# Performance work log

Hardware: AMD Instinct MI355X
Metric: run time of the kernel (lower is better)

Reference implementation:

```python
import jax, jax.numpy as jnp
import numpy as np

V, H, B, T = 32000, 512, 32, 64


def _gru(x, h0, Wih, Whh, bih, bhh):
    """PyTorch-style GRU, batch_first. x: [B,T,D], h0: [B,H]. Returns ([B,T,H], [B,H])."""
    # precompute input projections for all timesteps: [B,T,3H]
    xp = jnp.einsum('btd,gd->btg', x, Wih) + bih

    def step(h, xp_t):
        hp = h @ Whh.T + bhh                      # [B,3H]
        xr, xz, xn = jnp.split(xp_t, 3, axis=-1)
        hr, hz, hn = jnp.split(hp, 3, axis=-1)
        r = jax.nn.sigmoid(xr + hr)
        z = jax.nn.sigmoid(xz + hz)
        n = jnp.tanh(xn + r * hn)
        h_new = (1.0 - z) * n + z * h
        return h_new, h_new

    h_last, ys = jax.lax.scan(step, h0, jnp.swapaxes(xp, 0, 1))
    return jnp.swapaxes(ys, 0, 1), h_last


def setup_inputs() -> dict:
    key = jax.random.key(0)
    ks = jax.random.split(key, 12)
    s_emb = 1.0  # nn.Embedding default N(0,1)
    s_gru = 1.0 / np.sqrt(H)  # nn.GRU uniform(-1/sqrt(H), 1/sqrt(H))
    u = lambda k, shape, s: jax.random.uniform(k, shape, jnp.float32, -s, s)
    return {
        'input_seqs': jax.random.randint(ks[0], (B, T), 0, V),
        'target_seqs': jax.random.randint(ks[1], (B, T), 0, V),
        'enc_emb': jax.random.normal(ks[2], (V, H), jnp.float32) * s_emb,
        'enc_Wih': u(ks[3], (3 * H, H), s_gru),
        'enc_Whh': u(ks[4], (3 * H, H), s_gru),
        'enc_bih': u(ks[5], (3 * H,), s_gru),
        'enc_bhh': u(ks[6], (3 * H,), s_gru),
        'dec_emb': jax.random.normal(ks[7], (V, H), jnp.float32) * s_emb,
        'dec_Wih': u(ks[8], (3 * H, 2 * H), s_gru),
        'dec_Whh': u(ks[9], (3 * H, H), s_gru),
        'dec_bih': u(ks[10], (3 * H,), s_gru),
        'dec_bhh': u(ks[11], (3 * H,), s_gru),
        'out_W': u(jax.random.fold_in(key, 100), (V, H), s_gru),
        'out_b': u(jax.random.fold_in(key, 101), (V,), s_gru),
    }


def reference(input_seqs, target_seqs, enc_emb, enc_Wih, enc_Whh, enc_bih, enc_bhh,
              dec_emb, dec_Wih, dec_Whh, dec_bih, dec_bhh, out_W, out_b):
    b = input_seqs.shape[0]
    h0 = jnp.zeros((b, H), jnp.float32)
    # encoder: embed + single-layer GRU; thought = final hidden
    enc_x = enc_emb[input_seqs]                                  # [B,T,H]
    _, thought = _gru(enc_x, h0, enc_Wih, enc_Whh, enc_bih, enc_bhh)  # [B,H]
    # decoder: concat embedded target with broadcast thought along time
    dec_x = dec_emb[target_seqs]                                 # [B,T,H]
    t = dec_x.shape[1]
    rnn_in = jnp.concatenate([dec_x, jnp.broadcast_to(thought[:, None, :], (b, t, H))], axis=-1)
    rnn_in = jax.nn.relu(rnn_in)
    dec_out, _ = _gru(rnn_in, h0, dec_Wih, dec_Whh, dec_bih, dec_bhh)  # [B,T,H]
    logits = jnp.einsum('bth,vh->btv', dec_out, out_W) + out_b
    return jax.nn.log_softmax(logits, axis=-1)
```

## Files before the change

kernel.cpp:

```cpp
#include <hip/hip_runtime.h>
#include <hip/hip_bf16.h>
#include <cstdint>
#include <cstddef>

namespace {

constexpr int Hh = 512;
constexpr int G3 = 1536;
constexpr int Bb = 32;
constexpr int Tt = 64;
constexpr int Vv = 32000;

typedef __attribute__((ext_vector_type(8))) short short8;
typedef __attribute__((ext_vector_type(4))) float f32x4;
typedef unsigned long long ull;

__device__ __forceinline__ unsigned bf16bits(float f) {
  union { __hip_bfloat16 h; unsigned short u; } c;
  c.h = __float2bfloat16(f);
  return (unsigned)c.u;
}

__device__ __forceinline__ void gl_lds16(const void* g, void* l) {
  __builtin_amdgcn_global_load_lds(
      (const __attribute__((address_space(1))) unsigned int*)g,
      (__attribute__((address_space(3))) unsigned int*)l, 16, 0, 0);
}

__device__ __forceinline__ void cvt_range(const float* __restrict__ src,
                                          __hip_bfloat16* __restrict__ dst, int i, int n4) {
  if (i >= n4) return;
  float4 v = ((const float4*)src)[i];
  union { __hip_bfloat16 h[4]; uint2 u; } o;
  o.h[0] = __float2bfloat16(v.x);
  o.h[1] = __float2bfloat16(v.y);
  o.h[2] = __float2bfloat16(v.z);
  o.h[3] = __float2bfloat16(v.w);
  ((uint2*)dst)[i] = o.u;
}

__device__ __forceinline__ void pack_whh_core(const float* __restrict__ Whh,
                                              uint2* __restrict__ P, int k0, int i0) {
  __shared__ float tw[3][32][65];
  const int t = threadIdx.x;
  const int kk = t & 63, r4 = t >> 6;
  for (int ri = r4; ri < 96; ri += 4) {
    const int g = ri >> 5, ii = ri & 31;
    tw[g][ii][kk] = Whh[(size_t)(g * 512 + i0 + ii) * 512 + k0 + kk];
  }
  __syncthreads();
  const int ii = t & 31, kq = t >> 5;
  for (int k2 = kq; k2 < 64; k2 += 8) {
    unsigned rb = bf16bits(tw[0][ii][k2]);
    unsigned zb = bf16bits(tw[1][ii][k2]);
    unsigned nb = bf16bits(tw[2][ii][k2]);
    P[(size_t)(k0 + k2) * 512 + i0 + ii] = make_uint2((zb << 16) | rb, nb);
  }
}

__global__ __launch_bounds__(256) void prep_k(
    const float* __restrict__ enc_Wih, __hip_bfloat16* __restrict__ encWih_bf,
    const float* __restrict__ dec_Wih, __hip_bfloat16* __restrict__ decWih_bf,
    const float* __restrict__ enc_Whh, uint2* __restrict__ whhB_e,
    const float* __restrict__ dec_Whh, uint2* __restrict__ whhB_d,
    uint4* __restrict__ hTagZero) {
  const int blk = blockIdx.x;
  if (blk < 768) {
    cvt_range(enc_Wih, encWih_bf, blk * 256 + threadIdx.x, 1536 * 512 / 4);
  } else if (blk < 2304) {
    cvt_range(dec_Wih, decWih_bf, (blk - 768) * 256 + threadIdx.x, 1536 * 1024 / 4);
  } else if (blk < 2432) {
    const int b = blk - 2304;
    pack_whh_core(enc_Whh, whhB_e, (b & 7) * 64, (b >> 3) * 32);
  } else if (blk < 2560) {
    const int b = blk - 2432;
    pack_whh_core(dec_Whh, whhB_d, (b & 7) * 64, (b >> 3) * 32);
  } else {
    const int i = (blk - 2560) * 256 + threadIdx.x;
    hTagZero[i] = make_uint4(0u, 0u, 0u, 0u);
  }
}

__global__ void embed_k(const int* __restrict__ idx, const float* __restrict__ emb,
                        __hip_bfloat16* __restrict__ outp, int do_relu) {
  int row = blockIdx.x;
  int r = idx[row];
  float4 v = ((const float4*)(emb + (size_t)r * Hh))[threadIdx.x];
  if (do_relu) {
    v.x = fmaxf(v.x, 0.f); v.y = fmaxf(v.y, 0.f);
    v.z = fmaxf(v.z, 0.f); v.w = fmaxf(v.w, 0.f);
  }
  union { __hip_bfloat16 h[4]; uint2 u; } o;
  o.h[0] = __float2bfloat16(v.x);
  o.h[1] = __float2bfloat16(v.y);
  o.h[2] = __float2bfloat16(v.z);
  o.h[3] = __float2bfloat16(v.w);
  ((uint2*)(outp + (size_t)row * Hh))[threadIdx.x] = o.u;
}

__global__ __launch_bounds__(256) void gemm_bf16_k(
    const __hip_bfloat16* __restrict__ A,
    const __hip_bfloat16* __restrict__ B,
    float* __restrict__ C,
    __hip_bfloat16* __restrict__ Cbf,
    int lda, int ldb, int ldc, int K,
    const float* __restrict__ bias1,
    float2* __restrict__ partials,
    int ntm) {
  __shared__ __align__(16) char smem[32768];
  auto sA = (__hip_bfloat16(*)[64])smem;
  auto sB = (__hip_bfloat16(*)[64])(smem + 16384);

  const unsigned nwg = gridDim.x, gid = blockIdx.x;
  const unsigned q = nwg >> 3, r8 = nwg & 7, xc = gid & 7, jj = gid >> 3;
  const unsigned wg = (xc < r8 ? xc * (q + 1) : r8 * (q + 1) + (xc - r8) * q) + jj;
  const int m0 = (int)(wg % (unsigned)ntm) << 7;
  const int n0 = (int)(wg / (unsigned)ntm) << 7;

  const int tid = threadIdx.x;
  const int l = tid & 63, w = tid >> 6;
  const int wm = (w & 1) << 6, wn = (w >> 1) << 6;
  const int lr = l & 15;
  const int lk = (l >> 4) << 3;
  const int lrow = (w << 3) + (l >> 3);
  const int lcol = (l & 7) << 3;

  f32x4 acc[4][4];
  #pragma unroll
  for (int i = 0; i < 4; ++i)
    #pragma unroll
    for (int j = 0; j < 4; ++j) acc[i][j] = {0.f, 0.f, 0.f, 0.f};

  for (int k0 = 0; k0 < K; k0 += 64) {
    #pragma unroll
    for (int rr = 0; rr < 4; ++rr) {
      gl_lds16(A + (size_t)(m0 + (rr << 5) + lrow) * lda + k0 + lcol, &sA[(rr << 5) + (w << 3)][0]);
      gl_lds16(B + (size_t)(n0 + (rr << 5) + lrow) * ldb + k0 + lcol, &sB[(rr << 5) + (w << 3)][0]);
    }
    __syncthreads();
    #pragma unroll
    for (int kk = 0; kk < 64; kk += 32) {
      short8 aF[4], bF[4];
      #pragma unroll
      for (int ms = 0; ms < 4; ++ms) aF[ms] = *(const short8*)(&sA[wm + (ms << 4) + lr][kk + lk]);
      #pragma unroll
      for (int ns = 0; ns < 4; ++ns) bF[ns] = *(const short8*)(&sB[wn + (ns << 4) + lr][kk + lk]);
      #pragma unroll
      for (int ms = 0; ms < 4; ++ms)
        #pragma unroll
        for (int ns = 0; ns < 4; ++ns)
          acc[ms][ns] = __builtin_amdgcn_mfma_f32_16x16x32_bf16(aF[ms], bF[ns], acc[ms][ns], 0, 0, 0);
    }
    __syncthreads();
  }

  float* sg = (float*)smem + w * 1088;
  const int r2w = l >> 4;
  const int cw = l & 15;
  const int rbase = r2w << 2;
  #pragma unroll
  for (int ms = 0; ms < 4; ++ms) {
    #pragma unroll
    for (int ns = 0; ns < 4; ++ns)
      #pragma unroll
      for (int r = 0; r < 4; ++r) sg[(rbase + r) * 68 + (ns << 4) + lr] = acc[ms][ns][r];
    #pragma unroll
    for (int qq = 0; qq < 4; ++qq) {
      const int srow2 = (qq << 2) + r2w;
      float4 v = *(const float4*)&sg[srow2 * 68 + (cw << 2)];
      const int row = m0 + wm + (ms << 4) + srow2;
      const int col = n0 + wn + (cw << 2);
      if (bias1) {
        float4 b1 = *(const float4*)&bias1[col];
        v.x += b1.x; v.y += b1.y; v.z += b1.z; v.w += b1.w;
      }
      if (partials) {
        float m4 = fmaxf(fmaxf(v.x, v.y), fmaxf(v.z, v.w));
        #pragma unroll
        for (int hop = 1; hop < 16; hop <<= 1) m4 = fmaxf(m4, __shfl_xor(m4, hop));
        float e = __expf(v.x - m4) + __expf(v.y - m4) + __expf(v.z - m4) + __expf(v.w - m4);
        #pragma unroll
        for (int hop = 1; hop < 16; hop <<= 1) e += __shfl_xor(e, hop);
        if (cw == 0) partials[(size_t)row * 500 + ((n0 >> 6) + (wn >> 6))] = make_float2(m4, e);
        union { __hip_bfloat16 h[4]; uint2 u; } o;
        o.h[0] = __float2bfloat16(v.x);
        o.h[1] = __float2bfloat16(v.y);
        o.h[2] = __float2bfloat16(v.z);
        o.h[3] = __float2bfloat16(v.w);
        *(uint2*)&Cbf[(size_t)row * ldc + col] = o.u;
      } else {
        *(float4*)&C[(size_t)row * ldc + col] = v;
      }
    }
  }
}

__device__ __forceinline__ void gru_core(
    const int slice, const int bg,
    const float* __restrict__ xp, const uint2* __restrict__ whhB,
    const float* __restrict__ bhh,
    ull* __restrict__ hTag, __hip_bfloat16* __restrict__ dec_out,
    char* smem,
    const ull* __restrict__ thoughtTag,
    const float* __restrict__ decWih,
    const float* __restrict__ dec_bih) {
  float* sH = (float*)smem;
  float* sRed = (float*)(smem + 8192);
  const int tid = threadIdx.x;
  const int i0 = slice << 5;
  const int il = tid & 31, kc = tid >> 5;
  const int kb0 = kc << 5;

  float wrF[32], wzF[32], wnF[32];
  {
    const uint2* wp = whhB + i0 + il;
    #pragma unroll
    for (int k4 = 0; k4 < 8; ++k4) {
      #pragma unroll
      for (int j = 0; j < 4; ++j) {
        const int idx = (k4 << 2) + j;
        uint2 wv = wp[(size_t)(kb0 + idx) << 9];
        wrF[idx] = __uint_as_float(wv.x << 16);
        wzF[idx] = __uint_as_float(wv.x & 0xffff0000u);
        wnF[idx] = __uint_as_float(wv.y << 16);
      }
    }
  }

  float bh_r = 0.f, bh_z = 0.f, bh_n = 0.f;
  float tpr = 0.f, tpz = 0.f, tpn = 0.f;
  int gi = 0, bb = 0;
  if (tid < 128) {
    const int b = tid >> 5, i2 = tid & 31;
    gi = i0 + i2;
    bb = (bg << 2) + b;
    bh_r = bhh[gi]; bh_z = bhh[512 + gi]; bh_n = bhh[1024 + gi];
  }
  if (thoughtTag) {
    #pragma unroll
    for (int j = 0; j < 4; ++j) {
      ull v = __hip_atomic_load(thoughtTag + ((size_t)bg << 11) + (j << 9) + tid,
                                __ATOMIC_RELAXED, __HIP_MEMORY_SCOPE_AGENT);
      sH[(j << 9) + tid] = fmaxf(__uint_as_float((unsigned)v), 0.f);
    }
    __syncthreads();
    if (tid < 384) {
      const int b = tid / 96, j = tid % 96;
      const int g = j >> 5, i2 = j & 31;
      const int row = g * 512 + i0 + i2;
      const float4* w4 = (const float4*)(decWih + (size_t)row * 1024 + 512);
      const float* th = &sH[b << 9];
      float s = dec_bih[row];
      #pragma unroll 4
      for (int k = 0; k < 128; ++k) {
        float4 w = w4[k];
        float4 t4 = *(const float4*)&th[k << 2];
        s += w.x * t4.x + w.y * t4.y + w.z * t4.z + w.w * t4.w;
      }
      sRed[tid] = s;
    }
    __syncthreads();
    if (tid < 128) {
      const int b = tid >> 5, i2 = tid & 31;
      tpr = sRed[b * 96 + i2];
      tpz = sRed[b * 96 + 32 + i2];
      tpn = sRed[b * 96 + 64 + i2];
    }
    __syncthreads();
  }

  #pragma unroll 1
  for (int t = 0; t < Tt; ++t) {
    {
      const ull* hb = hTag + ((size_t)(t & 1) << 14) + ((size_t)bg << 11);
      #pragma unroll
      for (int j = 0; j < 4; ++j) {
        const ull* p = hb + (j << 9) + tid;
        ull v = __hip_atomic_load(p, __ATOMIC_RELAXED, __HIP_MEMORY_SCOPE_AGENT);
        while ((unsigned)(v >> 32) != (unsigned)t) {
          __builtin_amdgcn_s_sleep(1);
          v = __hip_atomic_load(p, __ATOMIC_RELAXED, __HIP_MEMORY_SCOPE_AGENT);
        }
        sH[(j << 9) + tid] = __uint_as_float((unsigned)v);
      }
    }
    __syncthreads();

    float a[12];
    #pragma unroll
    for (int v = 0; v < 12; ++v) a[v] = 0.f;
    #pragma unroll
    for (int k4 = 0; k4 < 8; ++k4) {
      const int kb = kb0 + (k4 << 2);
      float4 hv0 = *(const float4*)&sH[kb];
      float4 hv1 = *(const float4*)&sH[512 + kb];
      float4 hv2 = *(const float4*)&sH[1024 + kb];
      float4 hv3 = *(const float4*)&sH[1536 + kb];
      const float* h0p = (const float*)&hv0;
      const float* h1p = (const float*)&hv1;
      const float* h2p = (const float*)&hv2;
      const float* h3p = (const float*)&hv3;
      #pragma unroll
      for (int j = 0; j < 4; ++j) {
        const int idx = (k4 << 2) + j;
        const float wr = wrF[idx], wz = wzF[idx], wn = wnF[idx];
        a[0]  = fmaf(wr, h0p[j], a[0]);  a[1]  = fmaf(wz, h0p[j], a[1]);  a[2]  = fmaf(wn, h0p[j], a[2]);
        a[3]  = fmaf(wr, h1p[j], a[3]);  a[4]  = fmaf(wz, h1p[j], a[4]);  a[5]  = fmaf(wn, h1p[j], a[5]);
        a[6]  = fmaf(wr, h2p[j], a[6]);  a[7]  = fmaf(wz, h2p[j], a[7]);  a[8]  = fmaf(wn, h2p[j], a[8]);
        a[9]  = fmaf(wr, h3p[j], a[9]);  a[10] = fmaf(wz, h3p[j], a[10]); a[11] = fmaf(wn, h3p[j], a[11]);
      }
    }
    {
      float* red = &sRed[tid * 13];
      #pragma unroll
      for (int v = 0; v < 12; ++v) red[v] = a[v];
    }
    __syncthreads();

    if (tid < 128) {
      const int b = tid >> 5, i2 = tid & 31;
      float s0 = 0.f, s1 = 0.f, s2 = 0.f;
      #pragma unroll
      for (int kc2 = 0; kc2 < 16; ++kc2) {
        const float* rp = &sRed[(kc2 * 32 + i2) * 13 + b * 3];
        s0 += rp[0]; s1 += rp[1]; s2 += rp[2];
      }
      const float hr = s0 + bh_r;
      const float hz = s1 + bh_z;
      const float hn = s2 + bh_n;
      const size_t m = (size_t)bb * Tt + t;
      const float xr = xp[m * G3 + gi] + tpr;
      const float xz = xp[m * G3 + 512 + gi] + tpz;
      const float xn = xp[m * G3 + 1024 + gi] + tpn;
      const float rg = 1.f / (1.f + __expf(-(xr + hr)));
      const float zg = 1.f / (1.f + __expf(-(xz + hz)));
      const float ng = tanhf(xn + rg * hn);
      const float hnew = (1.f - zg) * ng + zg * sH[(b << 9) + gi];
      ull* dst = hTag + ((size_t)((t + 1) & 1) << 14) + ((size_t)bb << 9) + gi;
      __hip_atomic_store(dst, ((ull)(unsigned)(t + 1) << 32) | (ull)__float_as_uint(hnew),
                         __ATOMIC_RELAXED, __HIP_MEMORY_SCOPE_AGENT);
      if (dec_out) dec_out[((size_t)m << 9) + gi] = __float2bfloat16(hnew);
    }
    __syncthreads();
  }
}

__device__ __forceinline__ void gemm_tile_core(
    const int tid, const int m0, const int n0,
    const __hip_bfloat16* __restrict__ A, const __hip_bfloat16* __restrict__ B,
    float* __restrict__ C, int lda, int ldb, int ldc, int K, char* smem) {
  auto sA = (__hip_bfloat16(*)[64])smem;
  auto sB = (__hip_bfloat16(*)[64])(smem + 16384);
  const int l = tid & 63, w = tid >> 6;
  const int wm = (w & 1) << 6, wn = (w >> 1) << 6;
  const int lr = l & 15;
  const int lk = (l >> 4) << 3;
  const int lrow = (w << 3) + (l >> 3);
  const int lcol = (l & 7) << 3;

  f32x4 acc[4][4];
  #pragma unroll
  for (int i = 0; i < 4; ++i)
    #pragma unroll
    for (int j = 0; j < 4; ++j) acc[i][j] = {0.f, 0.f, 0.f, 0.f};

  for (int k0 = 0; k0 < K; k0 += 64) {
    #pragma unroll
    for (int rr = 0; rr < 4; ++rr) {
      gl_lds16(A + (size_t)(m0 + (rr << 5) + lrow) * lda + k0 + lcol, &sA[(rr << 5) + (w << 3)][0]);
      gl_lds16(B + (size_t)(n0 + (rr << 5) + lrow) * ldb + k0 + lcol, &sB[(rr << 5) + (w << 3)][0]);
    }
    __syncthreads();
    #pragma unroll
    for (int kk = 0; kk < 64; kk += 32) {
      short8 aF[4], bF[4];
      #pragma unroll
      for (int ms = 0; ms < 4; ++ms) aF[ms] = *(const short8*)(&sA[wm + (ms << 4) + lr][kk + lk]);
      #pragma unroll
      for (int ns = 0; ns < 4; ++ns) bF[ns] = *(const short8*)(&sB[wn + (ns << 4) + lr][kk + lk]);
      #pragma unroll
      for (int ms = 0; ms < 4; ++ms)
        #pragma unroll
        for (int ns = 0; ns < 4; ++ns)
          acc[ms][ns] = __builtin_amdgcn_mfma_f32_16x16x32_bf16(aF[ms], bF[ns], acc[ms][ns], 0, 0, 0);
    }
    __syncthreads();
  }

  float* sg = (float*)smem + w * 1088;
  const int r2w = l >> 4;
  const int cw = l & 15;
  const int rbase = r2w << 2;
  #pragma unroll
  for (int ms = 0; ms < 4; ++ms) {
    #pragma unroll
    for (int ns = 0; ns < 4; ++ns)
      #pragma unroll
      for (int r = 0; r < 4; ++r) sg[(rbase + r) * 68 + (ns << 4) + lr] = acc[ms][ns][r];
    #pragma unroll
    for (int qq = 0; qq < 4; ++qq) {
      const int srow2 = (qq << 2) + r2w;
      float4 v = *(const float4*)&sg[srow2 * 68 + (cw << 2)];
      *(float4*)&C[(size_t)(m0 + wm + (ms << 4) + srow2) * ldc + n0 + wn + (cw << 2)] = v;
    }
  }
}

__global__ __launch_bounds__(512, 1) void enc_fused_k(
    const float* __restrict__ enc_xp, const uint2* __restrict__ whhB_e,
    const float* __restrict__ enc_bhh, ull* __restrict__ hTag_e,
    const __hip_bfloat16* __restrict__ decX_bf, const __hip_bfloat16* __restrict__ decWih_bf,
    float* __restrict__ dec_xp,
    const float* __restrict__ out_W, __hip_bfloat16* __restrict__ outW_bf) {
  __shared__ __align__(16) char smem[65536];
  const int blk = blockIdx.x;
  if (blk < 128) {
    gru_core(blk & 15, blk >> 4, enc_xp, whhB_e, enc_bhh, hTag_e, nullptr, smem,
             nullptr, nullptr, nullptr);
  } else if (blk < 224) {
    const int half = threadIdx.x >> 8;
    const int tile = ((blk - 128) << 1) + half;
    const int m0 = (tile & 15) << 7;
    const int n0 = (tile >> 4) << 7;
    gemm_tile_core(threadIdx.x & 255, m0, n0, decX_bf, decWih_bf, dec_xp,
                   512, 1024, G3, 512, smem + (half << 15));
  } else {
    const int n4 = Vv * Hh / 4;
    for (int i = ((blk - 224) << 9) + threadIdx.x; i < n4; i += 16 * 512) {
      float4 v = ((const float4*)out_W)[i];
      union { __hip_bfloat16 h[4]; uint2 u; } o;
      o.h[0] = __float2bfloat16(v.x);
      o.h[1] = __float2bfloat16(v.y);
      o.h[2] = __float2bfloat16(v.z);
      o.h[3] = __float2bfloat16(v.w);
      ((uint2*)outW_bf)[i] = o.u;
    }
  }
}

__global__ __launch_bounds__(512, 1) void gru_dec_k(
    const float* __restrict__ xp, const uint2* __restrict__ whhB,
    const float* __restrict__ bhh,
    const ull* __restrict__ thoughtTag,
    const float* __restrict__ decWih, const float* __restrict__ dec_bih,
    ull* __restrict__ hTag, __hip_bfloat16* __restrict__ dec_out) {
  __shared__ __align__(16) char smem[34816];
  gru_core(blockIdx.x & 15, blockIdx.x >> 4, xp, whhB, bhh, hTag, dec_out, smem,
           thoughtTag, decWih, dec_bih);
}

__global__ __launch_bounds__(256) void lsm_final_k(float* __restrict__ X,
                                                   const float2* __restrict__ P) {
  const int row = blockIdx.x;
  const int tid = threadIdx.x;
  float m = -3.4e38f, s = 0.f;
  for (int j = tid; j < 500; j += 256) {
    float2 p = P[(size_t)row * 500 + j];
    if (p.x > m) { s = s * __expf(m - p.x) + p.y; m = p.x; }
    else         { s += p.y * __expf(p.x - m); }
  }
  #pragma unroll
  for (int off2 = 32; off2 > 0; off2 >>= 1) {
    float mo = __shfl_down(m, off2);
    float so = __shfl_down(s, off2);
    float M = fmaxf(m, mo);
    s = s * __expf(m - M) + so * __expf(mo - M);
    m = M;
  }
  __shared__ float sm[4], ss[4];
  if ((tid & 63) == 0) { sm[tid >> 6] = m; ss[tid >> 6] = s; }
  __syncthreads();
  const float M4 = fmaxf(fmaxf(sm[0], sm[1]), fmaxf(sm[2], sm[3]));
  const float S = ss[0] * __expf(sm[0] - M4) + ss[1] * __expf(sm[1] - M4) +
                  ss[2] * __expf(sm[2] - M4) + ss[3] * __expf(sm[3] - M4);
  const float c = M4 + __logf(S);
  float4* p4 = (float4*)(X + (size_t)row * Vv);
  for (int j = tid; j < Vv / 4; j += 256) {
    float4 v = p4[j];
    v.x -= c; v.y -= c; v.z -= c; v.w -= c;
    p4[j] = v;
  }
}

__global__ __launch_bounds__(256) void lsm_final2_k(float* __restrict__ X,
                                                    const __hip_bfloat16* __restrict__ L,
                                                    const float2* __restrict__ P) {
  const int row = blockIdx.x;
  const int tid = threadIdx.x;
  float m = -3.4e38f, s = 0.f;
  for (int j = tid; j < 500; j += 256) {
    float2 p = P[(size_t)row * 500 + j];
    if (p.x > m) { s = s * __expf(m - p.x) + p.y; m = p.x; }
    else         { s += p.y * __expf(p.x - m); }
  }
  #pragma unroll
  for (int off2 = 32; off2 > 0; off2 >>= 1) {
    float mo = __shfl_down(m, off2);
    float so = __shfl_down(s, off2);
    float M = fmaxf(m, mo);
    s = s * __expf(m - M) + so * __expf(mo - M);
    m = M;
  }
  __shared__ float sm[4], ss[4];
  if ((tid & 63) == 0) { sm[tid >> 6] = m; ss[tid >> 6] = s; }
  __syncthreads();
  const float M4 = fmaxf(fmaxf(sm[0], sm[1]), fmaxf(sm[2], sm[3]));
  const float S = ss[0] * __expf(sm[0] - M4) + ss[1] * __expf(sm[1] - M4) +
                  ss[2] * __expf(sm[2] - M4) + ss[3] * __expf(sm[3] - M4);
  const float c = M4 + __logf(S);
  const short8* p8 = (const short8*)(L + (size_t)row * Vv);
  float4* o4 = (float4*)(X + (size_t)row * Vv);
  for (int j = tid; j < Vv / 8; j += 256) {
    short8 sv = p8[j];
    float4 a, b;
    a.x = __uint_as_float(((unsigned)(unsigned short)sv[0]) << 16) - c;
    a.y = __uint_as_float(((unsigned)(unsigned short)sv[1]) << 16) - c;
    a.z = __uint_as_float(((unsigned)(unsigned short)sv[2]) << 16) - c;
    a.w = __uint_as_float(((unsigned)(unsigned short)sv[3]) << 16) - c;
    b.x = __uint_as_float(((unsigned)(unsigned short)sv[4]) << 16) - c;
    b.y = __uint_as_float(((unsigned)(unsigned short)sv[5]) << 16) - c;
    b.z = __uint_as_float(((unsigned)(unsigned short)sv[6]) << 16) - c;
    b.w = __uint_as_float(((unsigned)(unsigned short)sv[7]) << 16) - c;
    o4[(j << 1)] = a;
    o4[(j << 1) + 1] = b;
  }
}

}

extern "C" void kernel_launch(void* const* d_in, const int* in_sizes, int n_in,
                              void* d_out, int out_size, void* d_ws, size_t ws_size,
                              hipStream_t stream) {
  (void)in_sizes; (void)n_in; (void)out_size;
  const int*   in_seq  = (const int*)d_in[0];
  const int*   tgt_seq = (const int*)d_in[1];
  const float* enc_emb = (const float*)d_in[2];
  const float* enc_Wih = (const float*)d_in[3];
  const float* enc_Whh = (const float*)d_in[4];
  const float* enc_bih = (const float*)d_in[5];
  const float* enc_bhh = (const float*)d_in[6];
  const float* dec_emb = (const float*)d_in[7];
  const float* dec_Wih = (const float*)d_in[8];
  const float* dec_Whh = (const float*)d_in[9];
  const float* dec_bih = (const float*)d_in[10];
  const float* dec_bhh = (const float*)d_in[11];
  const float* out_W   = (const float*)d_in[12];
  const float* out_b   = (const float*)d_in[13];
  float* out = (float*)d_out;

  char* ws = (char*)d_ws;
  size_t off = 0;
  auto alloc = [&](size_t bytes) -> void* {
    void* p = (void*)(ws + off);
    off += (bytes + 255) & ~(size_t)255;
    return p;
  };
  uint2* whhB_e            = (uint2*)alloc((size_t)512 * 512 * 8);
  uint2* whhB_d            = (uint2*)alloc((size_t)512 * 512 * 8);
  __hip_bfloat16* encWih_bf = (__hip_bfloat16*)alloc((size_t)1536 * 512 * 2);
  __hip_bfloat16* decWih_bf = (__hip_bfloat16*)alloc((size_t)1536 * 1024 * 2);
  __hip_bfloat16* outW_bf   = (__hip_bfloat16*)alloc((size_t)32000 * 512 * 2);
  __hip_bfloat16* encX_bf   = (__hip_bfloat16*)alloc((size_t)2048 * 512 * 2);
  __hip_bfloat16* decX_bf   = (__hip_bfloat16*)alloc((size_t)2048 * 512 * 2);
  float* enc_xp            = (float*)alloc((size_t)2048 * 1536 * 4);
  float* dec_xp            = (float*)alloc((size_t)2048 * 1536 * 4);
  ull* hTag_e              = (ull*)alloc((size_t)2 * 32 * 512 * 8);
  ull* hTag_d              = (ull*)alloc((size_t)2 * 32 * 512 * 8);
  __hip_bfloat16* decOut_bf = (__hip_bfloat16*)alloc((size_t)2048 * 512 * 2);
  float2* partials         = (float2*)alloc((size_t)2048 * 500 * 8);
  __hip_bfloat16* logitsBf  = (__hip_bfloat16*)alloc((size_t)2048 * Vv * 2);
  const bool bfLogits = (off <= ws_size);

  prep_k<<<2688, 256, 0, stream>>>(enc_Wih, encWih_bf, dec_Wih, decWih_bf,
                                   enc_Whh, whhB_e, dec_Whh, whhB_d, (uint4*)hTag_e);

  embed_k<<<2048, 128, 0, stream>>>(in_seq, enc_emb, encX_bf, 0);
  embed_k<<<2048, 128, 0, stream>>>(tgt_seq, dec_emb, decX_bf, 1);

  gemm_bf16_k<<<192, 256, 0, stream>>>(encX_bf, encWih_bf, enc_xp, nullptr,
                                       512, 512, G3, 512, enc_bih, nullptr, 16);

  enc_fused_k<<<240, 512, 0, stream>>>(enc_xp, whhB_e, enc_bhh, hTag_e,
                                       decX_bf, decWih_bf, dec_xp, out_W, outW_bf);

  gru_dec_k<<<128, 512, 0, stream>>>(dec_xp, whhB_d, dec_bhh,
                                     hTag_e, dec_Wih, dec_bih, hTag_d, decOut_bf);

  if (bfLogits) {
    gemm_bf16_k<<<4000, 256, 0, stream>>>(decOut_bf, outW_bf, nullptr, logitsBf,
                                          512, 512, Vv, 512, out_b, partials, 16);
    lsm_final2_k<<<2048, 256, 0, stream>>>(out, logitsBf, partials);
  } else {
    gemm_bf16_k<<<4000, 256, 0, stream>>>(decOut_bf, outW_bf, out, nullptr,
                                          512, 512, Vv, 512, out_b, partials, 16);
    lsm_final_k<<<2048, 256, 0, stream>>>(out, partials);
  }
}
```

Baseline: 873.5 us.

## Overlap output-projection GEMM with decoder GRU via per-timestep completion counters

Fuses the decoder GRU and the vocabulary logits GEMM into one kernel. 128 blocks run the recurrence, and after each timestep they bump a per-step done counter. Another 128 blocks spin on these counters and compute logit tiles (with the softmax partials) as soon as the needed time-major rows of the decoder output are complete. Decoder output is stored time-major through atomic packed bf16 stores, so the GEMM can start before the recurrence finishes instead of waiting for a separate launch. The cost is spin-waiting, atomic loads for the A operand and possible contention with the latency-bound recurrent blocks.

```diff
diff --git a/kernel.cpp b/kernel.cpp
--- a/kernel.cpp
+++ b/kernel.cpp
@@ -63,7 +63,7 @@
     const float* __restrict__ dec_Wih, __hip_bfloat16* __restrict__ decWih_bf,
     const float* __restrict__ enc_Whh, uint2* __restrict__ whhB_e,
     const float* __restrict__ dec_Whh, uint2* __restrict__ whhB_d,
-    uint4* __restrict__ hTagZero) {
+    uint4* __restrict__ zeroBase) {
   const int blk = blockIdx.x;
   if (blk < 768) {
     cvt_range(enc_Wih, encWih_bf, blk * 256 + threadIdx.x, 1536 * 512 / 4);
@@ -77,7 +77,7 @@
     pack_whh_core(dec_Whh, whhB_d, (b & 7) * 64, (b >> 3) * 32);
   } else {
     const int i = (blk - 2560) * 256 + threadIdx.x;
-    hTagZero[i] = make_uint4(0u, 0u, 0u, 0u);
+    if (i < 32784) zeroBase[i] = make_uint4(0u, 0u, 0u, 0u);
   }
 }
 
@@ -102,10 +102,8 @@
     const __hip_bfloat16* __restrict__ A,
     const __hip_bfloat16* __restrict__ B,
     float* __restrict__ C,
-    __hip_bfloat16* __restrict__ Cbf,
     int lda, int ldb, int ldc, int K,
     const float* __restrict__ bias1,
-    float2* __restrict__ partials,
     int ntm) {
   __shared__ __align__(16) char smem[32768];
   auto sA = (__hip_bfloat16(*)[64])smem;
@@ -174,23 +172,7 @@
         float4 b1 = *(const float4*)&bias1[col];
         v.x += b1.x; v.y += b1.y; v.z += b1.z; v.w += b1.w;
       }
-      if (partials) {
-        float m4 = fmaxf(fmaxf(v.x, v.y), fmaxf(v.z, v.w));
-        #pragma unroll
-        for (int hop = 1; hop < 16; hop <<= 1) m4 = fmaxf(m4, __shfl_xor(m4, hop));
-        float e = __expf(v.x - m4) + __expf(v.y - m4) + __expf(v.z - m4) + __expf(v.w - m4);
-        #pragma unroll
-        for (int hop = 1; hop < 16; hop <<= 1) e += __shfl_xor(e, hop);
-        if (cw == 0) partials[(size_t)row * 500 + ((n0 >> 6) + (wn >> 6))] = make_float2(m4, e);
-        union { __hip_bfloat16 h[4]; uint2 u; } o;
-        o.h[0] = __float2bfloat16(v.x);
-        o.h[1] = __float2bfloat16(v.y);
-        o.h[2] = __float2bfloat16(v.z);
-        o.h[3] = __float2bfloat16(v.w);
-        *(uint2*)&Cbf[(size_t)row * ldc + col] = o.u;
-      } else {
-        *(float4*)&C[(size_t)row * ldc + col] = v;
-      }
+      *(float4*)&C[(size_t)row * ldc + col] = v;
     }
   }
 }
@@ -199,7 +181,8 @@
     const int slice, const int bg,
     const float* __restrict__ xp, const uint2* __restrict__ whhB,
     const float* __restrict__ bhh,
-    ull* __restrict__ hTag, __hip_bfloat16* __restrict__ dec_out,
+    ull* __restrict__ hTag, unsigned* __restrict__ decOutU,
+    unsigned* __restrict__ doneCnt,
     char* smem,
     const ull* __restrict__ thoughtTag,
     const float* __restrict__ decWih,
@@ -339,9 +322,20 @@
       ull* dst = hTag + ((size_t)((t + 1) & 1) << 14) + ((size_t)bb << 9) + gi;
       __hip_atomic_store(dst, ((ull)(unsigned)(t + 1) << 32) | (ull)__float_as_uint(hnew),
                          __ATOMIC_RELAXED, __HIP_MEMORY_SCOPE_AGENT);
-      if (dec_out) dec_out[((size_t)m << 9) + gi] = __float2bfloat16(hnew);
-    }
-    __syncthreads();
+      if (decOutU) {
+        unsigned bbits = bf16bits(hnew);
+        unsigned pbits = __shfl_down(bbits, 1);
+        if (!(tid & 1)) {
+          const int r2 = (t << 5) + bb;
+          __hip_atomic_store(decOutU + (((r2 << 9) + gi) >> 1), (pbits << 16) | bbits,
+                             __ATOMIC_RELAXED, __HIP_MEMORY_SCOPE_AGENT);
+        }
+      }
+    }
+    __syncthreads();
+    if (doneCnt && tid == 0) {
+      __hip_atomic_fetch_add(doneCnt + t, 1u, __ATOMIC_RELAXED, __HIP_MEMORY_SCOPE_AGENT);
+    }
   }
 }
 
@@ -406,6 +400,98 @@
   }
 }
 
+__device__ __forceinline__ void gemm_logits_core(
+    const int tid, const int m0, const int n0,
+    const ull* __restrict__ Au,
+    const __hip_bfloat16* __restrict__ B,
+    const float* __restrict__ out_b,
+    float* __restrict__ outF, __hip_bfloat16* __restrict__ outBf,
+    float2* __restrict__ partials, const int bfOut, char* smem) {
+  auto sA = (__hip_bfloat16(*)[64])smem;
+  auto sB = (__hip_bfloat16(*)[64])(smem + 16384);
+  const int l = tid & 63, w = tid >> 6;
+  const int wm = (w & 1) << 6, wn = (w >> 1) << 6;
+  const int lr = l & 15;
+  const int lk = (l >> 4) << 3;
+  const int lrow = (w << 3) + (l >> 3);
+  const int lcol = (l & 7) << 3;
+
+  f32x4 acc[4][4];
+  #pragma unroll
+  for (int i = 0; i < 4; ++i)
+    #pragma unroll
+    for (int j = 0; j < 4; ++j) acc[i][j] = {0.f, 0.f, 0.f, 0.f};
+
+  for (int k0 = 0; k0 < 512; k0 += 64) {
+    #pragma unroll
+    for (int rr = 0; rr < 4; ++rr) {
+      const int ar = m0 + (rr << 5) + lrow;
+      const size_t offs = ((size_t)(ar << 9) + k0 + lcol) >> 2;
+      ull u0 = __hip_atomic_load(Au + offs, __ATOMIC_RELAXED, __HIP_MEMORY_SCOPE_AGENT);
+      ull u1 = __hip_atomic_load(Au + offs + 1, __ATOMIC_RELAXED, __HIP_MEMORY_SCOPE_AGENT);
+      int4 av;
+      av.x = (int)(unsigned)u0; av.y = (int)(unsigned)(u0 >> 32);
+      av.z = (int)(unsigned)u1; av.w = (int)(unsigned)(u1 >> 32);
+      *(int4*)&sA[(rr << 5) + lrow][lcol] = av;
+      gl_lds16(B + (size_t)(n0 + (rr << 5) + lrow) * 512 + k0 + lcol, &sB[(rr << 5) + (w << 3)][0]);
+    }
+    __syncthreads();
+    #pragma unroll
+    for (int kk = 0; kk < 64; kk += 32) {
+      short8 aF[4], bF[4];
+      #pragma unroll
+      for (int ms = 0; ms < 4; ++ms) aF[ms] = *(const short8*)(&sA[wm + (ms << 4) + lr][kk + lk]);
+      #pragma unroll
+      for (int ns = 0; ns < 4; ++ns) bF[ns] = *(const short8*)(&sB[wn + (ns << 4) + lr][kk + lk]);
+      #pragma unroll
+      for (int ms = 0; ms < 4; ++ms)
+        #pragma unroll
+        for (int ns = 0; ns < 4; ++ns)
+          acc[ms][ns] = __builtin_amdgcn_mfma_f32_16x16x32_bf16(aF[ms], bF[ns], acc[ms][ns], 0, 0, 0);
+    }
+    __syncthreads();
+  }
+
+  float* sg = (float*)smem + w * 1088;
+  const int r2w = l >> 4;
+  const int cw = l & 15;
+  const int rbase = r2w << 2;
+  #pragma unroll
+  for (int ms = 0; ms < 4; ++ms) {
+    #pragma unroll
+    for (int ns = 0; ns < 4; ++ns)
+      #pragma unroll
+      for (int r = 0; r < 4; ++r) sg[(rbase + r) * 68 + (ns << 4) + lr] = acc[ms][ns][r];
+    #pragma unroll
+    for (int qq = 0; qq < 4; ++qq) {
+      const int srow2 = (qq << 2) + r2w;
+      float4 v = *(const float4*)&sg[srow2 * 68 + (cw << 2)];
+      const int r2a = m0 + wm + (ms << 4) + srow2;
+      const int mrow = ((r2a & 31) << 6) + (r2a >> 5);
+      const int col = n0 + wn + (cw << 2);
+      float4 b1 = *(const float4*)&out_b[col];
+      v.x += b1.x; v.y += b1.y; v.z += b1.z; v.w += b1.w;
+      float m4 = fmaxf(fmaxf(v.x, v.y), fmaxf(v.z, v.w));
+      #pragma unroll
+      for (int hop = 1; hop < 16; hop <<= 1) m4 = fmaxf(m4, __shfl_xor(m4, hop));
+      float e = __expf(v.x - m4) + __expf(v.y - m4) + __expf(v.z - m4) + __expf(v.w - m4);
+      #pragma unroll
+      for (int hop = 1; hop < 16; hop <<= 1) e += __shfl_xor(e, hop);
+      if (cw == 0) partials[(size_t)mrow * 500 + ((n0 >> 6) + (wn >> 6))] = make_float2(m4, e);
+      if (bfOut) {
+        union { __hip_bfloat16 h[4]; uint2 u; } o;
+        o.h[0] = __float2bfloat16(v.x);
+        o.h[1] = __float2bfloat16(v.y);
+        o.h[2] = __float2bfloat16(v.z);
+        o.h[3] = __float2bfloat16(v.w);
+        *(uint2*)&outBf[(size_t)mrow * Vv + col] = o.u;
+      } else {
+        *(float4*)&outF[(size_t)mrow * Vv + col] = v;
+      }
+    }
+  }
+}
+
 __global__ __launch_bounds__(512, 1) void enc_fused_k(
     const float* __restrict__ enc_xp, const uint2* __restrict__ whhB_e,
     const float* __restrict__ enc_bhh, ull* __restrict__ hTag_e,
@@ -415,7 +501,7 @@
   __shared__ __align__(16) char smem[65536];
   const int blk = blockIdx.x;
   if (blk < 128) {
-    gru_core(blk & 15, blk >> 4, enc_xp, whhB_e, enc_bhh, hTag_e, nullptr, smem,
+    gru_core(blk & 15, blk >> 4, enc_xp, whhB_e, enc_bhh, hTag_e, nullptr, nullptr, smem,
              nullptr, nullptr, nullptr);
   } else if (blk < 224) {
     const int half = threadIdx.x >> 8;
@@ -438,15 +524,41 @@
   }
 }
 
-__global__ __launch_bounds__(512, 1) void gru_dec_k(
-    const float* __restrict__ xp, const uint2* __restrict__ whhB,
-    const float* __restrict__ bhh,
-    const ull* __restrict__ thoughtTag,
-    const float* __restrict__ decWih, const float* __restrict__ dec_bih,
-    ull* __restrict__ hTag, __hip_bfloat16* __restrict__ dec_out) {
-  __shared__ __align__(16) char smem[34816];
-  gru_core(blockIdx.x & 15, blockIdx.x >> 4, xp, whhB, bhh, hTag, dec_out, smem,
-           thoughtTag, decWih, dec_bih);
+__global__ __launch_bounds__(512, 1) void dec_fused_k(
+    const float* __restrict__ dec_xp, const uint2* __restrict__ whhB_d,
+    const float* __restrict__ dec_bhh,
+    const ull* __restrict__ thoughtTag, const float* __restrict__ dec_Wih,
+    const float* __restrict__ dec_bih,
+    ull* __restrict__ hTag_d, unsigned* __restrict__ decOutU, unsigned* __restrict__ doneCnt,
+    const __hip_bfloat16* __restrict__ outW_bf, const float* __restrict__ out_b,
+    float* __restrict__ outF, __hip_bfloat16* __restrict__ logitsBf,
+    float2* __restrict__ partials, int bfOut) {
+  __shared__ __align__(16) char smem[65536];
+  const int blk = blockIdx.x;
+  if (blk < 128) {
+    gru_core(blk & 15, blk >> 4, dec_xp, whhB_d, dec_bhh, hTag_d, decOutU, doneCnt, smem,
+             thoughtTag, dec_Wih, dec_bih);
+  } else {
+    const int b = blk - 128;
+    const int tid = threadIdx.x;
+    #pragma unroll 1
+    for (int j = 0; j < 16; ++j) {
+      const int p = j * 128 + b;
+      if (p >= 2000) break;
+      const int mT = (2 * p + 1) / 250;
+      const int thi = 4 * mT + 3;
+      if (tid == 0) {
+        while (__hip_atomic_load(doneCnt + thi, __ATOMIC_RELAXED, __HIP_MEMORY_SCOPE_AGENT) < 128u)
+          __builtin_amdgcn_s_sleep(2);
+      }
+      __syncthreads();
+      const int half = tid >> 8;
+      const int tile = 2 * p + half;
+      gemm_logits_core(tid & 255, (tile / 250) << 7, (tile % 250) << 7,
+                       (const ull*)decOutU, outW_bf, out_b, outF, logitsBf,
+                       partials, bfOut, smem + (half << 15));
+    }
+  }
 }
 
 __global__ __launch_bounds__(256) void lsm_final_k(float* __restrict__ X,
@@ -566,33 +678,33 @@
   float* dec_xp            = (float*)alloc((size_t)2048 * 1536 * 4);
   ull* hTag_e              = (ull*)alloc((size_t)2 * 32 * 512 * 8);
   ull* hTag_d              = (ull*)alloc((size_t)2 * 32 * 512 * 8);
-  __hip_bfloat16* decOut_bf = (__hip_bfloat16*)alloc((size_t)2048 * 512 * 2);
+  unsigned* doneCnt        = (unsigned*)alloc((size_t)64 * 4);
+  unsigned* decOutU        = (unsigned*)alloc((size_t)2048 * 512 * 2);
   float2* partials         = (float2*)alloc((size_t)2048 * 500 * 8);
   __hip_bfloat16* logitsBf  = (__hip_bfloat16*)alloc((size_t)2048 * Vv * 2);
   const bool bfLogits = (off <= ws_size);
 
-  prep_k<<<2688, 256, 0, stream>>>(enc_Wih, encWih_bf, dec_Wih, decWih_bf,
+  prep_k<<<2689, 256, 0, stream>>>(enc_Wih, encWih_bf, dec_Wih, decWih_bf,
                                    enc_Whh, whhB_e, dec_Whh, whhB_d, (uint4*)hTag_e);
 
   embed_k<<<2048, 128, 0, stream>>>(in_seq, enc_emb, encX_bf, 0);
   embed_k<<<2048, 128, 0, stream>>>(tgt_seq, dec_emb, decX_bf, 1);
 
-  gemm_bf16_k<<<192, 256, 0, stream>>>(encX_bf, encWih_bf, enc_xp, nullptr,
-                                       512, 512, G3, 512, enc_bih, nullptr, 16);
+  gemm_bf16_k<<<192, 256, 0, stream>>>(encX_bf, encWih_bf, enc_xp,
+                                       512, 512, G3, 512, enc_bih, 16);
 
   enc_fused_k<<<240, 512, 0, stream>>>(enc_xp, whhB_e, enc_bhh, hTag_e,
                                        decX_bf, decWih_bf, dec_xp, out_W, outW_bf);
 
-  gru_dec_k<<<128, 512, 0, stream>>>(dec_xp, whhB_d, dec_bhh,
-                                     hTag_e, dec_Wih, dec_bih, hTag_d, decOut_bf);
+  dec_fused_k<<<256, 512, 0, stream>>>(dec_xp, whhB_d, dec_bhh,
+                                       hTag_e, dec_Wih, dec_bih,
+                                       hTag_d, decOutU, doneCnt,
+                                       outW_bf, out_b,
+                                       out, logitsBf, partials, bfLogits ? 1 : 0);
 
   if (bfLogits) {
-    gemm_bf16_k<<<4000, 256, 0, stream>>>(decOut_bf, outW_bf, nullptr, logitsBf,
-                                          512, 512, Vv, 512, out_b, partials, 16);
     lsm_final2_k<<<2048, 256, 0, stream>>>(out, logitsBf, partials);
   } else {
-    gemm_bf16_k<<<4000, 256, 0, stream>>>(decOut_bf, outW_bf, out, nullptr,
-                                          512, 512, Vv, 512, out_b, partials, 16);
     lsm_final_k<<<2048, 256, 0, stream>>>(out, partials);
   }
 }
```

Measured after the change: 887.4 us. No clear change (+1.6%).
